# Optimization experiments

Hardware: AMD Instinct MI355X
Metric: run time of the kernel (lower is better)

Reference implementation:

```python
import jax, jax.numpy as jnp
import numpy as np

NEG_INF = -1e9  # matches tf mask value -1000000000.0
LEAKY_ALPHA = 0.2  # tf.nn.leaky_relu default


def setup_inputs() -> dict:
    key = jax.random.key(0)
    k1, k2, k3, k4 = jax.random.split(key, 4)
    B, N, F, U = 8, 2048, 128, 128
    X = jax.random.normal(k1, (B, N, F), dtype=jnp.float32)
    A = jax.random.randint(k2, (B, N, N), 0, 2, dtype=jnp.int32)
    W = jax.random.normal(k3, (F, U), dtype=jnp.float32) * 0.1
    a = jax.random.normal(k4, (2 * U, 1), dtype=jnp.float32) * 0.1
    return {"X": X, "A": A, "W": W, "a": a}


def reference(X, A, W, a):
    # H = X @ W : [B, N, U]
    H = jnp.einsum('bnf,fu->bnu', X, W)
    U = H.shape[-1]
    # Additive decomposition of the tile+concat: [H_i || H_j] @ a = H_i@a_src + H_j@a_dst
    a_src = a[:U, 0]   # [U]
    a_dst = a[U:, 0]   # [U]
    s = H @ a_src      # [B, N]
    t = H @ a_dst      # [B, N]
    e = s[:, :, None] + t[:, None, :]            # [B, N, N] pairwise logits
    e = jax.nn.leaky_relu(e, negative_slope=LEAKY_ALPHA)
    mask = jnp.where(A > 0, 0.0, NEG_INF).astype(e.dtype)
    attention = jax.nn.softmax(e + mask, axis=-1)  # [B, N, N]
    H_out = jnp.einsum('bij,bju->biu', attention, H)
    return jax.nn.relu(H_out)
```

## Files before the change

### kernel.cpp

```cpp
#include <hip/hip_runtime.h>
#include <hip/hip_bf16.h>


#define NEG_INF -1.0e9f

typedef __bf16 bf16x8 __attribute__((ext_vector_type(8)));
typedef unsigned short ushort8 __attribute__((ext_vector_type(8)));
typedef float f32x4 __attribute__((ext_vector_type(4)));

__device__ __forceinline__ unsigned short f2b(float x) {
    unsigned u = __builtin_bit_cast(unsigned, x);
    u += 0x7fffu + ((u >> 16) & 1u);
    return (unsigned short)(u >> 16);
}

__device__ __forceinline__ void gload_lds16(const void* g, void* l) {
    __builtin_amdgcn_global_load_lds(
        (const __attribute__((address_space(1))) void*)g,
        (__attribute__((address_space(3))) void*)l, 16, 0, 0);
}

__global__ __launch_bounds__(256) void k_h(const float* __restrict__ X,
                                           const float* __restrict__ W,
                                           const float* __restrict__ a,
                                           unsigned short* __restrict__ HT,
                                           float* __restrict__ sbuf,
                                           float* __restrict__ tbuf) {
    __shared__ unsigned short WT[128 * 136];

    const int tid  = threadIdx.x;
    const int w    = tid >> 6;
    const int lane = tid & 63;
    const int r    = lane & 15;
    const int cg   = lane >> 4;

    for (int i = tid; i < 16384; i += 256) {
        int u = i >> 7, f = i & 127;
        WT[u * 136 + f] = f2b(W[f * 128 + u]);
    }
    __syncthreads();

    const int row0 = blockIdx.x * 64 + w * 16;
    const int b    = row0 >> 11;
    const int n0   = row0 & 2047;
    const int arow = row0 + r;

    f32x4 acc[8] = {};

#pragma unroll
    for (int k0 = 0; k0 < 128; k0 += 32) {
        const float* xp = X + (size_t)arow * 128 + k0 + cg * 8;
        ushort8 xa;
#pragma unroll
        for (int j = 0; j < 8; j++) xa[j] = f2b(xp[j]);
        bf16x8 av = __builtin_bit_cast(bf16x8, xa);
#pragma unroll
        for (int ut = 0; ut < 8; ut++) {
            ushort8 wb = *(const ushort8*)(&WT[(ut * 16 + r) * 136 + k0 + cg * 8]);
            acc[ut] = __builtin_amdgcn_mfma_f32_16x16x32_bf16(
                av, __builtin_bit_cast(bf16x8, wb), acc[ut], 0, 0, 0);
        }
    }

    float sp[4] = {0.f, 0.f, 0.f, 0.f};
    float tp[4] = {0.f, 0.f, 0.f, 0.f};
#pragma unroll
    for (int ut = 0; ut < 8; ut++) {
        int u = ut * 16 + r;
        float as = a[u];
        float ad = a[128 + u];
#pragma unroll
        for (int reg = 0; reg < 4; reg++) {
            float h = acc[ut][reg];
            int nrow = n0 + cg * 4 + reg;
            HT[((size_t)b * 128 + u) * 2048 + nrow] = f2b(h);
            sp[reg] += h * as;
            tp[reg] += h * ad;
        }
    }
#pragma unroll
    for (int msk = 1; msk < 16; msk <<= 1) {
#pragma unroll
        for (int reg = 0; reg < 4; reg++) {
            sp[reg] += __shfl_xor(sp[reg], msk);
            tp[reg] += __shfl_xor(tp[reg], msk);
        }
    }
    if (r == 0) {
#pragma unroll
        for (int reg = 0; reg < 4; reg++) {
            int row = row0 + cg * 4 + reg;
            sbuf[row] = sp[reg];
            tbuf[row] = tp[reg];
        }
    }
}

__global__ __launch_bounds__(512) void k_attn(const int* __restrict__ A,
                                              const unsigned short* __restrict__ HT,
                                              const float* __restrict__ sbuf,
                                              const float* __restrict__ tbuf,
                                              float* __restrict__ out) {
    __shared__ char smem[65536];
    __shared__ float dSm[4][64];

    const int tid  = threadIdx.x;
    const int w    = tid >> 6;
    const int lane = tid & 63;
    const int r    = lane & 15;
    const int cg   = lane >> 4;
    const int jq   = w >> 1;
    const int g    = w & 1;
    const int bid  = blockIdx.x;
    const int b    = bid & 7;
    const int it   = bid >> 3;
    const int i0   = it * 64;
    const int rot  = it & 15;

    const int irow0 = i0 + g * 32 + r;
    const float s0 = sbuf[b * 2048 + irow0];
    const float s1 = sbuf[b * 2048 + irow0 + 16];
    const unsigned short* Hb = HT + ((size_t)b * 128) * 2048 + jq * 512;
    const int*   Aq0 = A    + ((size_t)(b * 2048 + irow0)) * 2048 + jq * 512 + cg * 8;
    const int*   Aq1 = Aq0 + 16 * 2048;
    const float* Tq  = tbuf + (size_t)b * 2048 + jq * 512 + cg * 8;

    const int srow = (lane >> 2);
    const int csrc = (lane & 3) ^ ((lane >> 2) & 3) ^ ((lane >> 4) & 3);
    char* const qbase = smem + jq * 16384;
    const unsigned short* src0 = Hb + (size_t)(g * 64 + srow) * 2048 + csrc * 8;
    const int rsl = ((r & 3) ^ ((r >> 2) & 3));

    f32x4 acc0[8] = {};
    f32x4 acc1[8] = {};
    float den0 = 0.f, den1 = 0.f;

    int4   aP0[2][2], aP1[2][2];
    float4 tP[2][2];
    {
        const int j0 = rot * 32;
        const int j1 = ((1 + rot) & 15) * 32;
        aP0[0][0] = *(const int4*)(Aq0 + j0);
        aP0[0][1] = *(const int4*)(Aq0 + j0 + 4);
        aP1[0][0] = *(const int4*)(Aq1 + j0);
        aP1[0][1] = *(const int4*)(Aq1 + j0 + 4);
        tP[0][0]  = *(const float4*)(Tq + j0);
        tP[0][1]  = *(const float4*)(Tq + j0 + 4);
        aP0[1][0] = *(const int4*)(Aq0 + j1);
        aP0[1][1] = *(const int4*)(Aq0 + j1 + 4);
        aP1[1][0] = *(const int4*)(Aq1 + j1);
        aP1[1][1] = *(const int4*)(Aq1 + j1 + 4);
        tP[1][0]  = *(const float4*)(Tq + j1);
        tP[1][1]  = *(const float4*)(Tq + j1 + 4);
#pragma unroll
        for (int i = 0; i < 4; i++)
            gload_lds16(src0 + (size_t)i * 16 * 2048 + j0,
                        qbase + (g * 4 + i) * 1024);
    }
    __syncthreads();

#pragma unroll
    for (int k = 0; k < 16; ++k) {
        const int p = k & 1;

        int4   ca0 = aP0[p][0], ca1 = aP0[p][1];
        int4   cb0 = aP1[p][0], cb1 = aP1[p][1];
        float4 ct0 = tP[p][0],  ct1 = tP[p][1];

        if (k < 15) {
            const int jn = ((k + 1 + rot) & 15) * 32;
            char* dst = qbase + (p ^ 1) * 8192;
#pragma unroll
            for (int i = 0; i < 4; i++)
                gload_lds16(src0 + (size_t)i * 16 * 2048 + jn,
                            dst + (g * 4 + i) * 1024);
        }
        if (k < 14) {
            const int ja = ((k + 2 + rot) & 15) * 32;
            aP0[p][0] = *(const int4*)(Aq0 + ja);
            aP0[p][1] = *(const int4*)(Aq0 + ja + 4);
            aP1[p][0] = *(const int4*)(Aq1 + ja);
            aP1[p][1] = *(const int4*)(Aq1 + ja + 4);
            tP[p][0]  = *(const float4*)(Tq + ja);
            tP[p][1]  = *(const float4*)(Tq + ja + 4);
        }

        float tv[8] = {ct0.x, ct0.y, ct0.z, ct0.w, ct1.x, ct1.y, ct1.z, ct1.w};
        int   a0i[8] = {ca0.x, ca0.y, ca0.z, ca0.w, ca1.x, ca1.y, ca1.z, ca1.w};
        int   a1i[8] = {cb0.x, cb0.y, cb0.z, cb0.w, cb1.x, cb1.y, cb1.z, cb1.w};
        bf16x8 pa0, pa1;
#pragma unroll
        for (int jj = 0; jj < 8; jj++) {
            float x0 = s0 + tv[jj];
            float e0 = fmaxf(x0, 0.2f * x0);
            float p0 = __expf(e0 - 16.0f);
            p0 = a0i[jj] > 0 ? p0 : 0.f;
            den0 += p0;
            pa0[jj] = (__bf16)p0;

            float x1 = s1 + tv[jj];
            float e1 = fmaxf(x1, 0.2f * x1);
            float p1 = __expf(e1 - 16.0f);
            p1 = a1i[jj] > 0 ? p1 : 0.f;
            den1 += p1;
            pa1[jj] = (__bf16)p1;
        }

        if (k < 14)      asm volatile("s_waitcnt vmcnt(10)" ::: "memory");
        else if (k < 15) asm volatile("s_waitcnt vmcnt(4)" ::: "memory");
        else             asm volatile("s_waitcnt vmcnt(0)" ::: "memory");
        __builtin_amdgcn_s_barrier();
        __builtin_amdgcn_sched_barrier(0);

        const char* buf = qbase + p * 8192;
#pragma unroll
        for (int ut = 0; ut < 8; ut++) {
            ushort8 hb = *(const ushort8*)(buf + (ut * 16 + r) * 64 +
                                           ((cg ^ rsl) * 16));
            bf16x8 hbv = __builtin_bit_cast(bf16x8, hb);
            acc0[ut] = __builtin_amdgcn_mfma_f32_16x16x32_bf16(pa0, hbv, acc0[ut], 0, 0, 0);
            acc1[ut] = __builtin_amdgcn_mfma_f32_16x16x32_bf16(pa1, hbv, acc1[ut], 0, 0, 0);
        }

        if (k < 15) {
            __builtin_amdgcn_s_barrier();
            __builtin_amdgcn_sched_barrier(0);
        }
    }

    den0 += __shfl_xor(den0, 16);
    den0 += __shfl_xor(den0, 32);
    den1 += __shfl_xor(den1, 16);
    den1 += __shfl_xor(den1, 32);

    __syncthreads();

    if (cg == 0) { dSm[jq][g * 32 + r] = den0; dSm[jq][g * 32 + 16 + r] = den1; }

    float* accS = (float*)smem;
#pragma unroll
    for (int gg = 0; gg < 2; ++gg) {
        __syncthreads();
        if (g == gg && jq != 0) {
            const int base = (jq - 1) * 32;
#pragma unroll
            for (int ut = 0; ut < 8; ut++)
#pragma unroll
                for (int reg = 0; reg < 4; reg++) {
                    accS[(base + cg * 4 + reg) * 132 + ut * 16 + r]      = acc0[ut][reg];
                    accS[(base + 16 + cg * 4 + reg) * 132 + ut * 16 + r] = acc1[ut][reg];
                }
        }
        __syncthreads();
        if (g == gg && jq == 0) {
            float dinv0[4], dinv1[4];
#pragma unroll
            for (int reg = 0; reg < 4; reg++) {
                const int row0_ = gg * 32 + cg * 4 + reg;
                const int row1_ = gg * 32 + 16 + cg * 4 + reg;
                dinv0[reg] = 1.0f / (dSm[0][row0_] + dSm[1][row0_] +
                                     dSm[2][row0_] + dSm[3][row0_]);
                dinv1[reg] = 1.0f / (dSm[0][row1_] + dSm[1][row1_] +
                                     dSm[2][row1_] + dSm[3][row1_]);
            }
#pragma unroll
            for (int ut = 0; ut < 8; ut++) {
#pragma unroll
                for (int reg = 0; reg < 4; reg++) {
                    const int lr0 = cg * 4 + reg;
                    const int lr1 = 16 + cg * 4 + reg;
                    float n0 = acc0[ut][reg]
                             + accS[(0 * 32 + lr0) * 132 + ut * 16 + r]
                             + accS[(1 * 32 + lr0) * 132 + ut * 16 + r]
                             + accS[(2 * 32 + lr0) * 132 + ut * 16 + r];
                    float n1 = acc1[ut][reg]
                             + accS[(0 * 32 + lr1) * 132 + ut * 16 + r]
                             + accS[(1 * 32 + lr1) * 132 + ut * 16 + r]
                             + accS[(2 * 32 + lr1) * 132 + ut * 16 + r];
                    out[((size_t)(b * 2048 + i0 + gg * 32 + lr0)) * 128 +
                        ut * 16 + r] = fmaxf(n0 * dinv0[reg], 0.f);
                    out[((size_t)(b * 2048 + i0 + gg * 32 + lr1)) * 128 +
                        ut * 16 + r] = fmaxf(n1 * dinv1[reg], 0.f);
                }
            }
        }
    }
}

extern "C" void kernel_launch(void* const* d_in, const int* in_sizes, int n_in,
                              void* d_out, int out_size, void* d_ws, size_t ws_size,
                              hipStream_t stream) {
    const float* X = (const float*)d_in[0];
    const int*   A = (const int*)d_in[1];
    const float* W = (const float*)d_in[2];
    const float* a = (const float*)d_in[3];
    float* out = (float*)d_out;

    char* ws = (char*)d_ws;
    float*          sb  = (float*)(ws);
    float*          tb  = (float*)(ws + 65536);
    unsigned short* HT  = (unsigned short*)(ws + 131072);

    k_h<<<dim3(256), dim3(256), 0, stream>>>(X, W, a, HT, sb, tb);
    k_attn<<<dim3(256), dim3(512), 0, stream>>>(A, HT, sb, tb, out);
}
```

Measured before the change: 59.26 us.

## Double the attention kernel's j-tile to 64 columns with larger LDS staging

Each pipeline step now covers 64 j columns instead of 32, so the loop runs 8 iterations instead of 16, halving barrier and waitcnt overhead per unit of work. The LDS buffer doubles to 128 KB, with an 8-way XOR swizzle for the wider rows, and the mask/t prefetch registers double. Launch bounds request 2 blocks per CU. The cost is much higher register and LDS pressure; at 128 KB LDS per block, occupancy may fall to one block per CU, which could reduce latency hiding.

```diff
diff --git a/kernel.cpp b/kernel.cpp
--- a/kernel.cpp
+++ b/kernel.cpp
@@ -96,12 +96,12 @@
     }
 }
 
-__global__ __launch_bounds__(512) void k_attn(const int* __restrict__ A,
-                                              const unsigned short* __restrict__ HT,
-                                              const float* __restrict__ sbuf,
-                                              const float* __restrict__ tbuf,
-                                              float* __restrict__ out) {
-    __shared__ char smem[65536];
+__global__ __launch_bounds__(512, 2) void k_attn(const int* __restrict__ A,
+                                                 const unsigned short* __restrict__ HT,
+                                                 const float* __restrict__ sbuf,
+                                                 const float* __restrict__ tbuf,
+                                                 float* __restrict__ out) {
+    __shared__ char smem[131072];
     __shared__ float dSm[4][64];
 
     const int tid  = threadIdx.x;
@@ -115,7 +115,7 @@
     const int b    = bid & 7;
     const int it   = bid >> 3;
     const int i0   = it * 64;
-    const int rot  = it & 15;
+    const int rot  = it & 7;
 
     const int irow0 = i0 + g * 32 + r;
     const float s0 = sbuf[b * 2048 + irow0];
@@ -125,104 +125,132 @@
     const int*   Aq1 = Aq0 + 16 * 2048;
     const float* Tq  = tbuf + (size_t)b * 2048 + jq * 512 + cg * 8;
 
-    const int srow = (lane >> 2);
-    const int csrc = (lane & 3) ^ ((lane >> 2) & 3) ^ ((lane >> 4) & 3);
-    char* const qbase = smem + jq * 16384;
+    const int srow = (lane >> 3);
+    const int csrc = (lane & 7) ^ ((lane >> 3) & 7);
+    char* const qbase = smem + jq * 32768;
     const unsigned short* src0 = Hb + (size_t)(g * 64 + srow) * 2048 + csrc * 8;
-    const int rsl = ((r & 3) ^ ((r >> 2) & 3));
+    const int rxor = r & 7;
 
     f32x4 acc0[8] = {};
     f32x4 acc1[8] = {};
     float den0 = 0.f, den1 = 0.f;
 
-    int4   aP0[2][2], aP1[2][2];
-    float4 tP[2][2];
+    int4   aP0[2][4], aP1[2][4];
+    float4 tP[2][4];
     {
-        const int j0 = rot * 32;
-        const int j1 = ((1 + rot) & 15) * 32;
+        const int j0 = rot * 64;
+        const int j1 = ((1 + rot) & 7) * 64;
+#pragma unroll
+        for (int i = 0; i < 8; i++)
+            gload_lds16(src0 + (size_t)i * 8 * 2048 + j0,
+                        qbase + g * 8192 + i * 1024);
         aP0[0][0] = *(const int4*)(Aq0 + j0);
         aP0[0][1] = *(const int4*)(Aq0 + j0 + 4);
+        aP0[0][2] = *(const int4*)(Aq0 + j0 + 32);
+        aP0[0][3] = *(const int4*)(Aq0 + j0 + 36);
         aP1[0][0] = *(const int4*)(Aq1 + j0);
         aP1[0][1] = *(const int4*)(Aq1 + j0 + 4);
+        aP1[0][2] = *(const int4*)(Aq1 + j0 + 32);
+        aP1[0][3] = *(const int4*)(Aq1 + j0 + 36);
         tP[0][0]  = *(const float4*)(Tq + j0);
         tP[0][1]  = *(const float4*)(Tq + j0 + 4);
+        tP[0][2]  = *(const float4*)(Tq + j0 + 32);
+        tP[0][3]  = *(const float4*)(Tq + j0 + 36);
         aP0[1][0] = *(const int4*)(Aq0 + j1);
         aP0[1][1] = *(const int4*)(Aq0 + j1 + 4);
+        aP0[1][2] = *(const int4*)(Aq0 + j1 + 32);
+        aP0[1][3] = *(const int4*)(Aq0 + j1 + 36);
         aP1[1][0] = *(const int4*)(Aq1 + j1);
         aP1[1][1] = *(const int4*)(Aq1 + j1 + 4);
+        aP1[1][2] = *(const int4*)(Aq1 + j1 + 32);
+        aP1[1][3] = *(const int4*)(Aq1 + j1 + 36);
         tP[1][0]  = *(const float4*)(Tq + j1);
         tP[1][1]  = *(const float4*)(Tq + j1 + 4);
-#pragma unroll
-        for (int i = 0; i < 4; i++)
-            gload_lds16(src0 + (size_t)i * 16 * 2048 + j0,
-                        qbase + (g * 4 + i) * 1024);
+        tP[1][2]  = *(const float4*)(Tq + j1 + 32);
+        tP[1][3]  = *(const float4*)(Tq + j1 + 36);
     }
     __syncthreads();
 
 #pragma unroll
-    for (int k = 0; k < 16; ++k) {
+    for (int k = 0; k < 8; ++k) {
         const int p = k & 1;
 
-        int4   ca0 = aP0[p][0], ca1 = aP0[p][1];
-        int4   cb0 = aP1[p][0], cb1 = aP1[p][1];
-        float4 ct0 = tP[p][0],  ct1 = tP[p][1];
-
-        if (k < 15) {
-            const int jn = ((k + 1 + rot) & 15) * 32;
-            char* dst = qbase + (p ^ 1) * 8192;
-#pragma unroll
-            for (int i = 0; i < 4; i++)
-                gload_lds16(src0 + (size_t)i * 16 * 2048 + jn,
-                            dst + (g * 4 + i) * 1024);
-        }
-        if (k < 14) {
-            const int ja = ((k + 2 + rot) & 15) * 32;
+        float tv0[8] = {tP[p][0].x, tP[p][0].y, tP[p][0].z, tP[p][0].w,
+                        tP[p][1].x, tP[p][1].y, tP[p][1].z, tP[p][1].w};
+        float tv1[8] = {tP[p][2].x, tP[p][2].y, tP[p][2].z, tP[p][2].w,
+                        tP[p][3].x, tP[p][3].y, tP[p][3].z, tP[p][3].w};
+        int a00[8] = {aP0[p][0].x, aP0[p][0].y, aP0[p][0].z, aP0[p][0].w,
+                      aP0[p][1].x, aP0[p][1].y, aP0[p][1].z, aP0[p][1].w};
+        int a01[8] = {aP0[p][2].x, aP0[p][2].y, aP0[p][2].z, aP0[p][2].w,
+                      aP0[p][3].x, aP0[p][3].y, aP0[p][3].z, aP0[p][3].w};
+        int a10[8] = {aP1[p][0].x, aP1[p][0].y, aP1[p][0].z, aP1[p][0].w,
+                      aP1[p][1].x, aP1[p][1].y, aP1[p][1].z, aP1[p][1].w};
+        int a11[8] = {aP1[p][2].x, aP1[p][2].y, aP1[p][2].z, aP1[p][2].w,
+                      aP1[p][3].x, aP1[p][3].y, aP1[p][3].z, aP1[p][3].w};
+        bf16x8 pa00, pa01, pa10, pa11;
+#pragma unroll
+        for (int jj = 0; jj < 8; jj++) {
+            float x, e, pp;
+            x = s0 + tv0[jj]; e = fmaxf(x, 0.2f * x);
+            pp = __expf(e - 16.0f); pp = a00[jj] > 0 ? pp : 0.f;
+            den0 += pp; pa00[jj] = (__bf16)pp;
+            x = s0 + tv1[jj]; e = fmaxf(x, 0.2f * x);
+            pp = __expf(e - 16.0f); pp = a01[jj] > 0 ? pp : 0.f;
+            den0 += pp; pa01[jj] = (__bf16)pp;
+            x = s1 + tv0[jj]; e = fmaxf(x, 0.2f * x);
+            pp = __expf(e - 16.0f); pp = a10[jj] > 0 ? pp : 0.f;
+            den1 += pp; pa10[jj] = (__bf16)pp;
+            x = s1 + tv1[jj]; e = fmaxf(x, 0.2f * x);
+            pp = __expf(e - 16.0f); pp = a11[jj] > 0 ? pp : 0.f;
+            den1 += pp; pa11[jj] = (__bf16)pp;
+        }
+
+        if (k < 7) {
+            const int jn = ((k + 1 + rot) & 7) * 64;
+            char* dst = qbase + (p ^ 1) * 16384 + g * 8192;
+#pragma unroll
+            for (int i = 0; i < 8; i++)
+                gload_lds16(src0 + (size_t)i * 8 * 2048 + jn,
+                            dst + i * 1024);
+        }
+        __builtin_amdgcn_sched_barrier(0);
+        if (k < 6) {
+            const int ja = ((k + 2 + rot) & 7) * 64;
             aP0[p][0] = *(const int4*)(Aq0 + ja);
             aP0[p][1] = *(const int4*)(Aq0 + ja + 4);
+            aP0[p][2] = *(const int4*)(Aq0 + ja + 32);
+            aP0[p][3] = *(const int4*)(Aq0 + ja + 36);
             aP1[p][0] = *(const int4*)(Aq1 + ja);
             aP1[p][1] = *(const int4*)(Aq1 + ja + 4);
+            aP1[p][2] = *(const int4*)(Aq1 + ja + 32);
+            aP1[p][3] = *(const int4*)(Aq1 + ja + 36);
             tP[p][0]  = *(const float4*)(Tq + ja);
             tP[p][1]  = *(const float4*)(Tq + ja + 4);
-        }
-
-        float tv[8] = {ct0.x, ct0.y, ct0.z, ct0.w, ct1.x, ct1.y, ct1.z, ct1.w};
-        int   a0i[8] = {ca0.x, ca0.y, ca0.z, ca0.w, ca1.x, ca1.y, ca1.z, ca1.w};
-        int   a1i[8] = {cb0.x, cb0.y, cb0.z, cb0.w, cb1.x, cb1.y, cb1.z, cb1.w};
-        bf16x8 pa0, pa1;
-#pragma unroll
-        for (int jj = 0; jj < 8; jj++) {
-            float x0 = s0 + tv[jj];
-            float e0 = fmaxf(x0, 0.2f * x0);
-            float p0 = __expf(e0 - 16.0f);
-            p0 = a0i[jj] > 0 ? p0 : 0.f;
-            den0 += p0;
-            pa0[jj] = (__bf16)p0;
-
-            float x1 = s1 + tv[jj];
-            float e1 = fmaxf(x1, 0.2f * x1);
-            float p1 = __expf(e1 - 16.0f);
-            p1 = a1i[jj] > 0 ? p1 : 0.f;
-            den1 += p1;
-            pa1[jj] = (__bf16)p1;
-        }
-
-        if (k < 14)      asm volatile("s_waitcnt vmcnt(10)" ::: "memory");
-        else if (k < 15) asm volatile("s_waitcnt vmcnt(4)" ::: "memory");
-        else             asm volatile("s_waitcnt vmcnt(0)" ::: "memory");
+            tP[p][2]  = *(const float4*)(Tq + ja + 32);
+            tP[p][3]  = *(const float4*)(Tq + ja + 36);
+        }
+
+        if (k < 6)       asm volatile("s_waitcnt vmcnt(32)" ::: "memory");
+        else if (k == 6) asm volatile("s_waitcnt vmcnt(20)" ::: "memory");
+        else             asm volatile("s_waitcnt vmcnt(0)"  ::: "memory");
         __builtin_amdgcn_s_barrier();
         __builtin_amdgcn_sched_barrier(0);
 
-        const char* buf = qbase + p * 8192;
+        const char* buf = qbase + p * 16384;
 #pragma unroll
         for (int ut = 0; ut < 8; ut++) {
-            ushort8 hb = *(const ushort8*)(buf + (ut * 16 + r) * 64 +
-                                           ((cg ^ rsl) * 16));
-            bf16x8 hbv = __builtin_bit_cast(bf16x8, hb);
-            acc0[ut] = __builtin_amdgcn_mfma_f32_16x16x32_bf16(pa0, hbv, acc0[ut], 0, 0, 0);
-            acc1[ut] = __builtin_amdgcn_mfma_f32_16x16x32_bf16(pa1, hbv, acc1[ut], 0, 0, 0);
-        }
-
-        if (k < 15) {
+            const int base = (ut * 16 + r) * 128;
+            ushort8 h0 = *(const ushort8*)(buf + base + ((cg ^ rxor) * 16));
+            ushort8 h1 = *(const ushort8*)(buf + base + (((4 + cg) ^ rxor) * 16));
+            bf16x8 hb0 = __builtin_bit_cast(bf16x8, h0);
+            bf16x8 hb1 = __builtin_bit_cast(bf16x8, h1);
+            acc0[ut] = __builtin_amdgcn_mfma_f32_16x16x32_bf16(pa00, hb0, acc0[ut], 0, 0, 0);
+            acc0[ut] = __builtin_amdgcn_mfma_f32_16x16x32_bf16(pa01, hb1, acc0[ut], 0, 0, 0);
+            acc1[ut] = __builtin_amdgcn_mfma_f32_16x16x32_bf16(pa10, hb0, acc1[ut], 0, 0, 0);
+            acc1[ut] = __builtin_amdgcn_mfma_f32_16x16x32_bf16(pa11, hb1, acc1[ut], 0, 0, 0);
+        }
+
+        if (k < 7) {
             __builtin_amdgcn_s_barrier();
             __builtin_amdgcn_sched_barrier(0);
         }
```

Result: no change. 59.03 us (-0.4%).
